# Kernel optimization log

Hardware: AMD Instinct MI355X
Metric: run time of the kernel (lower is better)

The kernel has to match this reference:

```python
import jax, jax.numpy as jnp
import numpy as np

DIM = 512
NUM_HEADS = 8
HEAD_DIM = DIM // NUM_HEADS
LN_EPS = 1e-5


def setup_inputs() -> dict:
    key = jax.random.key(0)
    k1, k2, k3 = jax.random.split(key, 3)
    x = jax.random.normal(k1, (8, DIM, 32, 32), dtype=jnp.float32)
    # torch Linear default init scale ~ 1/sqrt(fan_in); keep values sane
    w_qkv = jax.random.normal(k2, (3 * DIM, DIM), dtype=jnp.float32) * (DIM ** -0.5)
    b_qkv = jax.random.normal(k3, (3 * DIM,), dtype=jnp.float32) * 0.01
    ln_gamma = jnp.ones((DIM,), dtype=jnp.float32)
    ln_beta = jnp.zeros((DIM,), dtype=jnp.float32)
    return {"x": x, "w_qkv": w_qkv, "b_qkv": b_qkv, "ln_gamma": ln_gamma, "ln_beta": ln_beta}


def _rotate_half(t):
    t1, t2 = jnp.split(t, 2, axis=-1)
    return jnp.concatenate((-t2, t1), axis=-1)


def reference(x, w_qkv, b_qkv, ln_gamma, ln_beta):
    B, C, H, W = x.shape
    N = H * W
    nh, hd = NUM_HEADS, HEAD_DIM
    scale = hd ** -0.5

    # [B, N, C]
    xt = x.reshape(B, C, N).transpose(0, 2, 1)

    # LayerNorm over channel dim
    mu = jnp.mean(xt, axis=-1, keepdims=True)
    var = jnp.mean(jnp.square(xt - mu), axis=-1, keepdims=True)
    xn = (xt - mu) * jax.lax.rsqrt(var + LN_EPS) * ln_gamma + ln_beta

    # QKV projection: [B, N, 3C]
    qkv = xn @ w_qkv.T + b_qkv
    qkv = qkv.reshape(B, N, 3, nh, hd).transpose(2, 0, 3, 1, 4)  # [3, B, nh, N, hd]
    q, k, v = qkv[0], qkv[1], qkv[2]

    # RoPE tables
    freqs = 1.0 / (10000.0 ** (jnp.arange(0, hd, 2, dtype=jnp.float32) / hd))
    pos = jnp.arange(N, dtype=jnp.float32)
    sinusoid = jnp.einsum('i,j->ij', pos, freqs)  # [N, hd/2]
    sin = jnp.repeat(jnp.sin(sinusoid), 2, axis=-1)[None, None]  # [1,1,N,hd]
    cos = jnp.repeat(jnp.cos(sinusoid), 2, axis=-1)[None, None]

    q = q * cos + _rotate_half(q) * sin
    k = k * cos + _rotate_half(k) * sin

    # Full softmax attention: [B, nh, N, N]
    attn = jnp.einsum('bhqd,bhkd->bhqk', q, k) * scale
    attn = jax.nn.softmax(attn, axis=-1)
    out = jnp.einsum('bhqk,bhkd->bhqd', attn, v)  # [B, nh, N, hd]

    out = out.transpose(0, 2, 1, 3).reshape(B, N, C)  # [B, N, C]
    # dropout=0 (eval): identity
    return out.transpose(0, 2, 1).reshape(B, C, H, W)
```

## Files before the change

### kernel.cpp

```cpp
#include <hip/hip_runtime.h>
#include <hip/hip_bf16.h>
#include <math.h>

using bf16 = __hip_bfloat16;
typedef __attribute__((ext_vector_type(8))) short short8;
typedef __attribute__((ext_vector_type(4))) float floatx4;
typedef __attribute__((ext_vector_type(4))) unsigned int uint4_;
typedef __attribute__((ext_vector_type(2))) unsigned int uint2_;

#define C_DIM   512
#define N_TOK   1024
#define NHEAD   8
#define HDIM    64
#define LN_EPSF 1e-5f

__device__ __forceinline__ unsigned short f2b(float f) {
    union { float f; unsigned int u; } v; v.f = f;
    unsigned int r = v.u + 0x7FFFu + ((v.u >> 16) & 1u);
    return (unsigned short)(r >> 16);
}
__device__ __forceinline__ float b2f(unsigned short u) {
    union { unsigned int i; float f; } v; v.i = ((unsigned int)u) << 16; return v.f;
}
__device__ __forceinline__ unsigned int cvt_pk_bf16(float lo, float hi) {
    unsigned int r;
    asm("v_cvt_pk_bf16_f32 %0, %1, %2" : "=v"(r) : "v"(lo), "v"(hi));
    return r;
}
__device__ __forceinline__ float fast_exp2(float x) {
    return __builtin_amdgcn_exp2f(x);
}

__global__ __launch_bounds__(256) void lnx_kernel(
        const float* __restrict__ x, const float* __restrict__ w,
        const float* __restrict__ gamma, const float* __restrict__ beta,
        float* __restrict__ sc, unsigned short* __restrict__ wf,
        unsigned short* __restrict__ xnf) {
    __shared__ float xs[C_DIM][36];
    __shared__ float red_s[8][32];
    __shared__ float red_q[8][32];
    __shared__ float muL[32], rsL[32];

    const int bx = blockIdx.x;
    const int t  = threadIdx.x;

    if (bx < 256) {
        const int b  = bx >> 5;
        const int n0 = (bx & 31) * 32;
        const float* xb = x + (size_t)b * C_DIM * N_TOK;

        #pragma unroll
        for (int i = 0; i < 16; ++i) {
            const int flat = i * 256 + t;
            const int c  = flat >> 3;
            const int f4 = flat & 7;
            const float4 v = *(const float4*)(xb + (size_t)c * N_TOK + n0 + f4 * 4);
            *(float4*)&xs[c][f4 * 4] = v;
        }
        __syncthreads();

        const int tl = t & 31, cg = t >> 5;
        float s = 0.f, q = 0.f;
        #pragma unroll 8
        for (int i2 = 0; i2 < 64; ++i2) {
            const float v = xs[cg * 64 + i2][tl];
            s += v; q += v * v;
        }
        red_s[cg][tl] = s; red_q[cg][tl] = q;
        __syncthreads();
        if (t < 32) {
            float S = 0.f, Q = 0.f;
            #pragma unroll
            for (int g2 = 0; g2 < 8; ++g2) { S += red_s[g2][t]; Q += red_q[g2][t]; }
            const float m   = S * (1.0f / C_DIM);
            const float var = Q * (1.0f / C_DIM) - m * m;
            muL[t] = m; rsL[t] = rsqrtf(var + LN_EPSF);
        }
        __syncthreads();

        const int wv   = t >> 6;
        const int lane = t & 63;
        const int cfr  = lane & 15;
        const int quad = lane >> 4;
        #pragma unroll
        for (int gg = 0; gg < 2; ++gg) {
            const int tloc = gg * 16 + cfr;
            const float m = muL[tloc], r = rsL[tloc];
            const int g16 = b * 64 + (n0 >> 4) + gg;
            #pragma unroll
            for (int kk = 0; kk < 4; ++kk) {
                const int kt  = wv * 4 + kk;
                const int ch0 = kt * 32 + quad * 8;
                const float4 g0 = *(const float4*)(gamma + ch0);
                const float4 g1 = *(const float4*)(gamma + ch0 + 4);
                const float4 b0 = *(const float4*)(beta + ch0);
                const float4 b1 = *(const float4*)(beta + ch0 + 4);
                float vv[8];
                #pragma unroll
                for (int j = 0; j < 8; ++j) vv[j] = (xs[ch0 + j][tloc] - m) * r;
                uint4_ pk;
                pk.x = cvt_pk_bf16(vv[0] * g0.x + b0.x, vv[1] * g0.y + b0.y);
                pk.y = cvt_pk_bf16(vv[2] * g0.z + b0.z, vv[3] * g0.w + b0.w);
                pk.z = cvt_pk_bf16(vv[4] * g1.x + b1.x, vv[5] * g1.y + b1.y);
                pk.w = cvt_pk_bf16(vv[6] * g1.z + b1.z, vv[7] * g1.w + b1.w);
                *(uint4_*)(xnf + (((size_t)g16 * 16 + kt) * 64 + lane) * 8) = pk;
            }
        }
    } else if (bx < 384) {
        const int idx = (bx - 256) * 256 + t;
        const int n = idx >> 5, f = idx & 31;
        const float fr = __expf((float)f * (-9.210340371976184f / 32.0f));
        float sv, cv;
        sincosf((float)n * fr, &sv, &cv);
        ((float2*)sc)[idx] = make_float2(sv, cv);
    } else {
        const int id   = (bx - 384) * 256 + t;
        const int lane = id & 63;
        const int ksl  = (id >> 6) & 15;
        const int j16  = id >> 10;
        const int c    = lane & 15;
        const int quad = lane >> 4;
        const float* wp = w + (size_t)(j16 * 16 + c) * C_DIM + ksl * 32 + quad * 8;
        const float4 w0 = *(const float4*)(wp);
        const float4 w1 = *(const float4*)(wp + 4);
        uint4_ pk;
        pk.x = cvt_pk_bf16(w0.x, w0.y);
        pk.y = cvt_pk_bf16(w0.z, w0.w);
        pk.z = cvt_pk_bf16(w1.x, w1.y);
        pk.w = cvt_pk_bf16(w1.z, w1.w);
        *(uint4_*)(wf + (size_t)id * 8) = pk;
    }
}

__global__ __launch_bounds__(256) void qkv_mfma_kernel(
        const unsigned short* __restrict__ xnf, const unsigned short* __restrict__ wf,
        const float* __restrict__ bias, const float* __restrict__ sc,
        unsigned short* __restrict__ qfr, unsigned short* __restrict__ kfr,
        unsigned short* __restrict__ vfr) {
    __shared__ short Es[4][64][72];

    const int t    = threadIdx.x;
    const int wv   = t >> 6;
    const int lane = t & 63;
    const int cl   = lane & 15;
    const int quad = lane >> 4;
    const int t0   = blockIdx.x * 128 + (wv & 1) * 64;
    const int j0w  = blockIdx.y * 128 + (wv >> 1) * 64;
    const int which = j0w >> 9;
    const int h     = (j0w >> 6) & 7;
    const int b     = t0 >> 10;
    const int n0q   = t0 & 1023;
    const int bh    = b * NHEAD + h;

    const unsigned short* ap = xnf + (size_t)(t0 >> 4) * 8192 + lane * 8;
    const unsigned short* bp = wf  + (size_t)(j0w >> 4) * 8192 + lane * 8;

    floatx4 acc[4][4];
    #pragma unroll
    for (int i = 0; i < 4; ++i)
        #pragma unroll
        for (int j = 0; j < 4; ++j) acc[i][j] = (floatx4){0.f, 0.f, 0.f, 0.f};

    #pragma unroll 2
    for (int kt = 0; kt < 16; ++kt) {
        short8 af[4], bfr[4];
        #pragma unroll
        for (int tt = 0; tt < 4; ++tt) af[tt]  = *(const short8*)(ap + ((size_t)tt * 16 + kt) * 512);
        #pragma unroll
        for (int jt = 0; jt < 4; ++jt) bfr[jt] = *(const short8*)(bp + ((size_t)jt * 16 + kt) * 512);
        #pragma unroll
        for (int tt = 0; tt < 4; ++tt)
            #pragma unroll
            for (int jt = 0; jt < 4; ++jt)
                acc[tt][jt] = __builtin_amdgcn_mfma_f32_16x16x32_bf16(af[tt], bfr[jt], acc[tt][jt], 0, 0, 0);
    }

    const float os = (which == 0) ? 0.125f : 1.0f;
    float bj[4];
    #pragma unroll
    for (int jt = 0; jt < 4; ++jt) bj[jt] = bias[j0w + jt * 16 + cl] * os;
    #pragma unroll
    for (int tt = 0; tt < 4; ++tt)
        #pragma unroll
        for (int jt = 0; jt < 4; ++jt)
            #pragma unroll
            for (int r = 0; r < 4; ++r)
                Es[wv][tt * 16 + quad * 4 + r][jt * 16 + cl] = (short)f2b(fmaf(acc[tt][jt][r], os, bj[jt]));

    if (which == 2) {
        unsigned short* vfb = vfr + ((size_t)bh * 16 + (n0q >> 6)) * 4096;
        #pragma unroll
        for (int dt = 0; dt < 4; ++dt) {
            #pragma unroll
            for (int ks = 0; ks < 2; ++ks) {
                short8 pk;
                #pragma unroll
                for (int j = 0; j < 8; ++j)
                    pk[j] = Es[wv][ks * 32 + quad * 8 + j][dt * 16 + cl];
                *(short8*)(vfb + (((size_t)dt * 2 + ks) * 64 + lane) * 8) = pk;
            }
        }
    } else {
        unsigned short* base = (which == 0)
            ? qfr + ((size_t)bh * 64 + (n0q >> 4)) * 1024
            : kfr + ((size_t)bh * 16 + (n0q >> 6)) * 4096;
        #pragma unroll
        for (int mt = 0; mt < 4; ++mt) {
            const int n = n0q + mt * 16 + cl;
            const float* scp = sc + ((size_t)n * 32 + quad * 4) * 2;
            #pragma unroll
            for (int ks = 0; ks < 2; ++ks) {
                const short8 v8 = *(const short8*)&Es[wv][mt * 16 + cl][ks * 32 + quad * 8];
                const short8 p8 = *(const short8*)&Es[wv][mt * 16 + cl][(ks ^ 1) * 32 + quad * 8];
                const float* sp = scp + ks * 32;
                const float4 s0 = *(const float4*)sp;
                const float4 s1 = *(const float4*)(sp + 4);
                const float sv[4] = {s0.x, s0.z, s1.x, s1.z};
                const float cv[4] = {s0.y, s0.w, s1.y, s1.w};
                const float sgn = ks ? 1.0f : -1.0f;
                uint4_ pk;
                unsigned int pw[4];
                #pragma unroll
                for (int f = 0; f < 4; ++f) {
                    const float svs = sgn * sv[f];
                    const float a0 = b2f((unsigned short)v8[2 * f]);
                    const float a1 = b2f((unsigned short)v8[2 * f + 1]);
                    const float p0 = b2f((unsigned short)p8[2 * f]);
                    const float p1 = b2f((unsigned short)p8[2 * f + 1]);
                    pw[f] = cvt_pk_bf16(fmaf(p0, svs, a0 * cv[f]),
                                        fmaf(p1, svs, a1 * cv[f]));
                }
                pk.x = pw[0]; pk.y = pw[1]; pk.z = pw[2]; pk.w = pw[3];
                *(uint4_*)(base + (((size_t)mt * 2 + ks) * 64 + lane) * 8) = pk;
            }
        }
    }
}

__global__ __launch_bounds__(256, 2) void attn_mfma_kernel(
        const unsigned short* __restrict__ qfr, const unsigned short* __restrict__ kfr,
        const unsigned short* __restrict__ vfr, float* __restrict__ out) {
    __shared__ __align__(16) short Plds[4][2][16][72];

    const int t    = threadIdx.x;
    const int wv   = t >> 6;
    const int lane = t & 63;
    const int c    = lane & 15;
    const int quad = lane >> 4;
    const int i    = blockIdx.x;
    const int bh   = (i & 7) * 8 + ((i >> 3) & 7);
    const int q32  = (i >> 6) * 4 + wv;
    const int b    = bh >> 3, h = bh & 7;

    const unsigned short* qp   = qfr + ((size_t)bh * 64 + q32 * 2) * 1024 + lane * 8;
    const unsigned short* kraw = kfr + (size_t)bh * 65536 + lane * 8;
    const unsigned short* vraw = vfr + (size_t)bh * 65536 + lane * 8;

    short8 qf[2][2];
    qf[0][0] = *(const short8*)(qp);
    qf[0][1] = *(const short8*)(qp + 512);
    qf[1][0] = *(const short8*)(qp + 1024);
    qf[1][1] = *(const short8*)(qp + 1536);

    floatx4 o_acc[4][2];
    float l_acc[2] = {0.f, 0.f};
    #pragma unroll
    for (int dt = 0; dt < 4; ++dt) {
        o_acc[dt][0] = (floatx4){0.f, 0.f, 0.f, 0.f};
        o_acc[dt][1] = (floatx4){0.f, 0.f, 0.f, 0.f};
    }

    const float LOG2E  = 1.4426950408889634f;
    const float ESHIFT = -23.083120654223414f;

    short8 kfA[4][2], vfA[4][2], kfB[4][2], vfB[4][2];

    auto loadf = [&](short8 (&kf)[4][2], short8 (&vf)[4][2], int kt) {
        const unsigned short* kc = kraw + (size_t)kt * 4096;
        const unsigned short* vc = vraw + (size_t)kt * 4096;
        #pragma unroll
        for (int mt = 0; mt < 4; ++mt)
            #pragma unroll
            for (int ks = 0; ks < 2; ++ks) {
                kf[mt][ks] = *(const short8*)(kc + (mt * 2 + ks) * 512);
                vf[mt][ks] = *(const short8*)(vc + (mt * 2 + ks) * 512);
            }
    };

    auto step = [&](short8 (&kf)[4][2], short8 (&vf)[4][2]) {
        floatx4 st[4][2];
        __builtin_amdgcn_s_setprio(1);
        #pragma unroll
        for (int mt = 0; mt < 4; ++mt)
            #pragma unroll
            for (int u = 0; u < 2; ++u) {
                floatx4 z = (floatx4){0.f, 0.f, 0.f, 0.f};
                z = __builtin_amdgcn_mfma_f32_16x16x32_bf16(kf[mt][0], qf[u][0], z, 0, 0, 0);
                st[mt][u] = __builtin_amdgcn_mfma_f32_16x16x32_bf16(kf[mt][1], qf[u][1], z, 0, 0, 0);
            }
        __builtin_amdgcn_s_setprio(0);

        #pragma unroll
        for (int u = 0; u < 2; ++u)
            #pragma unroll
            for (int mt = 0; mt < 4; ++mt) {
                const float e0 = fast_exp2(fmaf(st[mt][u][0], LOG2E, ESHIFT));
                const float e1 = fast_exp2(fmaf(st[mt][u][1], LOG2E, ESHIFT));
                const float e2 = fast_exp2(fmaf(st[mt][u][2], LOG2E, ESHIFT));
                const float e3 = fast_exp2(fmaf(st[mt][u][3], LOG2E, ESHIFT));
                l_acc[u] += (e0 + e1) + (e2 + e3);
                uint2_ pk;
                pk.x = cvt_pk_bf16(e0, e1);
                pk.y = cvt_pk_bf16(e2, e3);
                *(uint2_*)&Plds[wv][u][c][mt * 16 + quad * 4] = pk;
            }

        #pragma unroll
        for (int u = 0; u < 2; ++u) {
            const short8 pf0 = *(const short8*)&Plds[wv][u][c][quad * 8];
            const short8 pf1 = *(const short8*)&Plds[wv][u][c][32 + quad * 8];
            __builtin_amdgcn_s_setprio(1);
            #pragma unroll
            for (int dt = 0; dt < 4; ++dt) {
                o_acc[dt][u] = __builtin_amdgcn_mfma_f32_16x16x32_bf16(vf[dt][0], pf0, o_acc[dt][u], 0, 0, 0);
                o_acc[dt][u] = __builtin_amdgcn_mfma_f32_16x16x32_bf16(vf[dt][1], pf1, o_acc[dt][u], 0, 0, 0);
            }
            __builtin_amdgcn_s_setprio(0);
        }
    };

    loadf(kfA, vfA, 0);
    #pragma unroll 1
    for (int kt = 0; kt < 16; kt += 2) {
        loadf(kfB, vfB, kt + 1);
        step(kfA, vfA);
        if (kt + 2 < 16) loadf(kfA, vfA, kt + 2);
        step(kfB, vfB);
    }

    #pragma unroll
    for (int u = 0; u < 2; ++u) {
        float l = l_acc[u];
        l += __shfl_xor(l, 16);
        l += __shfl_xor(l, 32);
        const float inv = 1.0f / l;
        const int qcol = (q32 * 2 + u) * 16 + c;
        #pragma unroll
        for (int dt = 0; dt < 4; ++dt)
            #pragma unroll
            for (int r = 0; r < 4; ++r) {
                const int d = dt * 16 + quad * 4 + r;
                out[((size_t)b * C_DIM + h * HDIM + d) * N_TOK + qcol] = o_acc[dt][u][r] * inv;
            }
    }
}

extern "C" void kernel_launch(void* const* d_in, const int* in_sizes, int n_in,
                              void* d_out, int out_size, void* d_ws, size_t ws_size,
                              hipStream_t stream) {
    const float* x     = (const float*)d_in[0];
    const float* w     = (const float*)d_in[1];
    const float* bias  = (const float*)d_in[2];
    const float* gamma = (const float*)d_in[3];
    const float* beta  = (const float*)d_in[4];
    float* out = (float*)d_out;

    char* ws = (char*)d_ws;
    unsigned short* qfr = (unsigned short*)(ws + 65536);
    unsigned short* kfr = (unsigned short*)(ws + 65536 + 8388608);
    unsigned short* vfr = (unsigned short*)(ws + 65536 + 16777216);
    unsigned short* xnf = (unsigned short*)(ws + 65536 + 25165824);
    unsigned short* wf  = (unsigned short*)(ws + 65536 + 33554432);
    float* sc           = (float*)(ws + 65536 + 35127296);

    hipLaunchKernelGGL(lnx_kernel, dim3(768), dim3(256), 0, stream,
                       x, w, gamma, beta, sc, wf, xnf);
    hipLaunchKernelGGL(qkv_mfma_kernel, dim3(64, 12), dim3(256), 0, stream,
                       xnf, wf, bias, sc, qfr, kfr, vfr);
    hipLaunchKernelGGL(attn_mfma_kernel, dim3(512), dim3(256), 0, stream, qfr, kfr, vfr, out);
}
```

Measured before the change: 125.6 us.

## Stage K/V tiles into LDS via global_load_lds double buffering in attention

The attention kernel previously had every wave load the full K and V fragments for each 64-key tile straight from global memory into registers, so the four waves of a block fetched the same data four times. Now each wave loads a quarter of the tile with direct global-to-LDS loads into a double-buffered shared-memory tile, and all waves read their fragments from LDS, with a block barrier after each tile. This cuts redundant global/L2 traffic and register pressure, but adds LDS reads, more shared memory per block (which may limit occupancy) and per-iteration __syncthreads. The QKV GEMM loop also raises wave priority around its MFMA block.

```diff
diff --git a/kernel.cpp b/kernel.cpp
--- a/kernel.cpp
+++ b/kernel.cpp
@@ -29,6 +29,11 @@
 }
 __device__ __forceinline__ float fast_exp2(float x) {
     return __builtin_amdgcn_exp2f(x);
+}
+typedef __attribute__((address_space(3))) void lds_void;
+typedef const __attribute__((address_space(1))) void gbl_void;
+__device__ __forceinline__ void gl16(const void* g, void* l) {
+    __builtin_amdgcn_global_load_lds((gbl_void*)g, (lds_void*)l, 16, 0, 0);
 }
 
 __global__ __launch_bounds__(256) void lnx_kernel(
@@ -168,11 +173,13 @@
         for (int tt = 0; tt < 4; ++tt) af[tt]  = *(const short8*)(ap + ((size_t)tt * 16 + kt) * 512);
         #pragma unroll
         for (int jt = 0; jt < 4; ++jt) bfr[jt] = *(const short8*)(bp + ((size_t)jt * 16 + kt) * 512);
+        __builtin_amdgcn_s_setprio(1);
         #pragma unroll
         for (int tt = 0; tt < 4; ++tt)
             #pragma unroll
             for (int jt = 0; jt < 4; ++jt)
                 acc[tt][jt] = __builtin_amdgcn_mfma_f32_16x16x32_bf16(af[tt], bfr[jt], acc[tt][jt], 0, 0, 0);
+        __builtin_amdgcn_s_setprio(0);
     }
 
     const float os = (which == 0) ? 0.125f : 1.0f;
@@ -240,6 +247,8 @@
 __global__ __launch_bounds__(256, 2) void attn_mfma_kernel(
         const unsigned short* __restrict__ qfr, const unsigned short* __restrict__ kfr,
         const unsigned short* __restrict__ vfr, float* __restrict__ out) {
+    __shared__ __align__(16) short kbuf[2][4096];
+    __shared__ __align__(16) short vbuf[2][4096];
     __shared__ __align__(16) short Plds[4][2][16][72];
 
     const int t    = threadIdx.x;
@@ -253,8 +262,8 @@
     const int b    = bh >> 3, h = bh & 7;
 
     const unsigned short* qp   = qfr + ((size_t)bh * 64 + q32 * 2) * 1024 + lane * 8;
-    const unsigned short* kraw = kfr + (size_t)bh * 65536 + lane * 8;
-    const unsigned short* vraw = vfr + (size_t)bh * 65536 + lane * 8;
+    const unsigned short* kraw = kfr + (size_t)bh * 65536;
+    const unsigned short* vraw = vfr + (size_t)bh * 65536;
 
     short8 qf[2][2];
     qf[0][0] = *(const short8*)(qp);
@@ -273,32 +282,32 @@
     const float LOG2E  = 1.4426950408889634f;
     const float ESHIFT = -23.083120654223414f;
 
-    short8 kfA[4][2], vfA[4][2], kfB[4][2], vfB[4][2];
-
-    auto loadf = [&](short8 (&kf)[4][2], short8 (&vf)[4][2], int kt) {
+    auto stage = [&](int kt, int cur) {
         const unsigned short* kc = kraw + (size_t)kt * 4096;
         const unsigned short* vc = vraw + (size_t)kt * 4096;
         #pragma unroll
-        for (int mt = 0; mt < 4; ++mt)
-            #pragma unroll
-            for (int ks = 0; ks < 2; ++ks) {
-                kf[mt][ks] = *(const short8*)(kc + (mt * 2 + ks) * 512);
-                vf[mt][ks] = *(const short8*)(vc + (mt * 2 + ks) * 512);
-            }
+        for (int s2 = 0; s2 < 2; ++s2) {
+            const int seg = wv * 2 + s2;
+            gl16(kc + seg * 512 + lane * 8, &kbuf[cur][seg * 512]);
+            gl16(vc + seg * 512 + lane * 8, &vbuf[cur][seg * 512]);
+        }
     };
 
-    auto step = [&](short8 (&kf)[4][2], short8 (&vf)[4][2]) {
+    auto step = [&](int cur) {
         floatx4 st[4][2];
-        __builtin_amdgcn_s_setprio(1);
-        #pragma unroll
-        for (int mt = 0; mt < 4; ++mt)
+        #pragma unroll
+        for (int mt = 0; mt < 4; ++mt) {
+            const short8 k0 = *(const short8*)&kbuf[cur][((mt * 2 + 0) * 64 + lane) * 8];
+            const short8 k1 = *(const short8*)&kbuf[cur][((mt * 2 + 1) * 64 + lane) * 8];
+            __builtin_amdgcn_s_setprio(1);
             #pragma unroll
             for (int u = 0; u < 2; ++u) {
                 floatx4 z = (floatx4){0.f, 0.f, 0.f, 0.f};
-                z = __builtin_amdgcn_mfma_f32_16x16x32_bf16(kf[mt][0], qf[u][0], z, 0, 0, 0);
-                st[mt][u] = __builtin_amdgcn_mfma_f32_16x16x32_bf16(kf[mt][1], qf[u][1], z, 0, 0, 0);
-            }
-        __builtin_amdgcn_s_setprio(0);
+                z = __builtin_amdgcn_mfma_f32_16x16x32_bf16(k0, qf[u][0], z, 0, 0, 0);
+                st[mt][u] = __builtin_amdgcn_mfma_f32_16x16x32_bf16(k1, qf[u][1], z, 0, 0, 0);
+            }
+            __builtin_amdgcn_s_setprio(0);
+        }
 
         #pragma unroll
         for (int u = 0; u < 2; ++u)
@@ -322,20 +331,23 @@
             __builtin_amdgcn_s_setprio(1);
             #pragma unroll
             for (int dt = 0; dt < 4; ++dt) {
-                o_acc[dt][u] = __builtin_amdgcn_mfma_f32_16x16x32_bf16(vf[dt][0], pf0, o_acc[dt][u], 0, 0, 0);
-                o_acc[dt][u] = __builtin_amdgcn_mfma_f32_16x16x32_bf16(vf[dt][1], pf1, o_acc[dt][u], 0, 0, 0);
+                const short8 v0 = *(const short8*)&vbuf[cur][((dt * 2 + 0) * 64 + lane) * 8];
+                const short8 v1 = *(const short8*)&vbuf[cur][((dt * 2 + 1) * 64 + lane) * 8];
+                o_acc[dt][u] = __builtin_amdgcn_mfma_f32_16x16x32_bf16(v0, pf0, o_acc[dt][u], 0, 0, 0);
+                o_acc[dt][u] = __builtin_amdgcn_mfma_f32_16x16x32_bf16(v1, pf1, o_acc[dt][u], 0, 0, 0);
             }
             __builtin_amdgcn_s_setprio(0);
         }
     };
 
-    loadf(kfA, vfA, 0);
+    stage(0, 0);
+    __syncthreads();
     #pragma unroll 1
-    for (int kt = 0; kt < 16; kt += 2) {
-        loadf(kfB, vfB, kt + 1);
-        step(kfA, vfA);
-        if (kt + 2 < 16) loadf(kfA, vfA, kt + 2);
-        step(kfB, vfB);
+    for (int kt = 0; kt < 16; ++kt) {
+        const int cur = kt & 1;
+        if (kt < 15) stage(kt + 1, cur ^ 1);
+        step(cur);
+        __syncthreads();
     }
 
     #pragma unroll
```

New measurement: 127.0 us. About the same (+1.1%).

## Double-buffer QKV GEMM operands via async global-to-LDS loads; fuse LN stats into load

Applied to the files above, without the earlier changes.

The QKV MFMA kernel now stages the A and B fragment tiles for each k-step into a double-buffered LDS region using global_load_lds. Each tile is loaded once per block and shared by the waves, rather than every wave reading it from global memory, and the next k-step's load overlaps the current MFMAs. MFMA sections are wrapped in s_setprio. LDS is reused for the epilogue staging. Separately, the LayerNorm kernel accumulates sums and sums of squares while loading x and reduces them with warp shuffles, replacing a second pass over shared memory. The price is a block barrier on every k-step and unroll 1.

```diff
diff --git a/kernel.cpp b/kernel.cpp
--- a/kernel.cpp
+++ b/kernel.cpp
@@ -29,6 +29,11 @@
 }
 __device__ __forceinline__ float fast_exp2(float x) {
     return __builtin_amdgcn_exp2f(x);
+}
+typedef __attribute__((address_space(3))) void lds_void;
+typedef const __attribute__((address_space(1))) void gbl_void;
+__device__ __forceinline__ void gl16(const void* g, void* l) {
+    __builtin_amdgcn_global_load_lds((gbl_void*)g, (lds_void*)l, 16, 0, 0);
 }
 
 __global__ __launch_bounds__(256) void lnx_kernel(
@@ -37,8 +42,8 @@
         float* __restrict__ sc, unsigned short* __restrict__ wf,
         unsigned short* __restrict__ xnf) {
     __shared__ float xs[C_DIM][36];
-    __shared__ float red_s[8][32];
-    __shared__ float red_q[8][32];
+    __shared__ float redw_s[4][8][4];
+    __shared__ float redw_q[4][8][4];
     __shared__ float muL[32], rsL[32];
 
     const int bx = blockIdx.x;
@@ -49,6 +54,7 @@
         const int n0 = (bx & 31) * 32;
         const float* xb = x + (size_t)b * C_DIM * N_TOK;
 
+        float s4[4] = {0.f, 0.f, 0.f, 0.f}, q4[4] = {0.f, 0.f, 0.f, 0.f};
         #pragma unroll
         for (int i = 0; i < 16; ++i) {
             const int flat = i * 256 + t;
@@ -56,30 +62,40 @@
             const int f4 = flat & 7;
             const float4 v = *(const float4*)(xb + (size_t)c * N_TOK + n0 + f4 * 4);
             *(float4*)&xs[c][f4 * 4] = v;
-        }
-        __syncthreads();
-
-        const int tl = t & 31, cg = t >> 5;
-        float s = 0.f, q = 0.f;
-        #pragma unroll 8
-        for (int i2 = 0; i2 < 64; ++i2) {
-            const float v = xs[cg * 64 + i2][tl];
-            s += v; q += v * v;
-        }
-        red_s[cg][tl] = s; red_q[cg][tl] = q;
+            s4[0] += v.x; q4[0] += v.x * v.x;
+            s4[1] += v.y; q4[1] += v.y * v.y;
+            s4[2] += v.z; q4[2] += v.z * v.z;
+            s4[3] += v.w; q4[3] += v.w * v.w;
+        }
+        #pragma unroll
+        for (int m = 8; m <= 32; m <<= 1)
+            #pragma unroll
+            for (int j = 0; j < 4; ++j) {
+                s4[j] += __shfl_xor(s4[j], m);
+                q4[j] += __shfl_xor(q4[j], m);
+            }
+        const int wv = t >> 6, lane = t & 63;
+        if (lane < 8) {
+            #pragma unroll
+            for (int j = 0; j < 4; ++j) {
+                redw_s[wv][lane][j] = s4[j];
+                redw_q[wv][lane][j] = q4[j];
+            }
+        }
         __syncthreads();
         if (t < 32) {
             float S = 0.f, Q = 0.f;
             #pragma unroll
-            for (int g2 = 0; g2 < 8; ++g2) { S += red_s[g2][t]; Q += red_q[g2][t]; }
+            for (int w2 = 0; w2 < 4; ++w2) {
+                S += redw_s[w2][t >> 2][t & 3];
+                Q += redw_q[w2][t >> 2][t & 3];
+            }
             const float m   = S * (1.0f / C_DIM);
             const float var = Q * (1.0f / C_DIM) - m * m;
             muL[t] = m; rsL[t] = rsqrtf(var + LN_EPSF);
         }
         __syncthreads();
 
-        const int wv   = t >> 6;
-        const int lane = t & 63;
         const int cfr  = lane & 15;
         const int quad = lane >> 4;
         #pragma unroll
@@ -137,23 +153,38 @@
         const float* __restrict__ bias, const float* __restrict__ sc,
         unsigned short* __restrict__ qfr, unsigned short* __restrict__ kfr,
         unsigned short* __restrict__ vfr) {
-    __shared__ short Es[4][64][72];
+    __shared__ __align__(16) char smem[36864];
+    short* stg = (short*)smem;
+    short (*Es)[72] = (short(*)[72])smem;
 
     const int t    = threadIdx.x;
     const int wv   = t >> 6;
     const int lane = t & 63;
     const int cl   = lane & 15;
     const int quad = lane >> 4;
-    const int t0   = blockIdx.x * 128 + (wv & 1) * 64;
-    const int j0w  = blockIdx.y * 128 + (wv >> 1) * 64;
+    const int tb   = blockIdx.x * 128;
+    const int jb   = blockIdx.y * 128;
+    const int t0   = tb + (wv & 1) * 64;
+    const int j0w  = jb + (wv >> 1) * 64;
     const int which = j0w >> 9;
     const int h     = (j0w >> 6) & 7;
     const int b     = t0 >> 10;
     const int n0q   = t0 & 1023;
     const int bh    = b * NHEAD + h;
-
-    const unsigned short* ap = xnf + (size_t)(t0 >> 4) * 8192 + lane * 8;
-    const unsigned short* bp = wf  + (size_t)(j0w >> 4) * 8192 + lane * 8;
+    const int g16b  = tb >> 4;
+    const int j16b  = jb >> 4;
+
+    auto stage = [&](int kt, int cur) {
+        short* dst = stg + cur * 8192;
+        #pragma unroll
+        for (int s = 0; s < 4; ++s) {
+            const int id = wv * 4 + s;
+            const unsigned short* src = (id < 8)
+                ? xnf + (size_t)(g16b + id) * 8192 + kt * 512 + lane * 8
+                : wf  + (size_t)(j16b + (id - 8)) * 8192 + kt * 512 + lane * 8;
+            gl16(src, dst + id * 512);
+        }
+    };
 
     floatx4 acc[4][4];
     #pragma unroll
@@ -161,19 +192,29 @@
         #pragma unroll
         for (int j = 0; j < 4; ++j) acc[i][j] = (floatx4){0.f, 0.f, 0.f, 0.f};
 
-    #pragma unroll 2
+    stage(0, 0);
+    #pragma unroll 1
     for (int kt = 0; kt < 16; ++kt) {
+        const int cur = kt & 1;
+        __syncthreads();
+        if (kt < 15) stage(kt + 1, cur ^ 1);
+        const short* base = stg + cur * 8192;
         short8 af[4], bfr[4];
         #pragma unroll
-        for (int tt = 0; tt < 4; ++tt) af[tt]  = *(const short8*)(ap + ((size_t)tt * 16 + kt) * 512);
-        #pragma unroll
-        for (int jt = 0; jt < 4; ++jt) bfr[jt] = *(const short8*)(bp + ((size_t)jt * 16 + kt) * 512);
+        for (int tt = 0; tt < 4; ++tt)
+            af[tt]  = *(const short8*)(base + ((wv & 1) * 4 + tt) * 512 + lane * 8);
+        #pragma unroll
+        for (int jt = 0; jt < 4; ++jt)
+            bfr[jt] = *(const short8*)(base + (8 + (wv >> 1) * 4 + jt) * 512 + lane * 8);
+        __builtin_amdgcn_s_setprio(1);
         #pragma unroll
         for (int tt = 0; tt < 4; ++tt)
             #pragma unroll
             for (int jt = 0; jt < 4; ++jt)
                 acc[tt][jt] = __builtin_amdgcn_mfma_f32_16x16x32_bf16(af[tt], bfr[jt], acc[tt][jt], 0, 0, 0);
-    }
+        __builtin_amdgcn_s_setprio(0);
+    }
+    __syncthreads();
 
     const float os = (which == 0) ? 0.125f : 1.0f;
     float bj[4];
@@ -185,7 +226,7 @@
         for (int jt = 0; jt < 4; ++jt)
             #pragma unroll
             for (int r = 0; r < 4; ++r)
-                Es[wv][tt * 16 + quad * 4 + r][jt * 16 + cl] = (short)f2b(fmaf(acc[tt][jt][r], os, bj[jt]));
+                Es[wv * 64 + tt * 16 + quad * 4 + r][jt * 16 + cl] = (short)f2b(fmaf(acc[tt][jt][r], os, bj[jt]));
 
     if (which == 2) {
         unsigned short* vfb = vfr + ((size_t)bh * 16 + (n0q >> 6)) * 4096;
@@ -196,7 +237,7 @@
                 short8 pk;
                 #pragma unroll
                 for (int j = 0; j < 8; ++j)
-                    pk[j] = Es[wv][ks * 32 + quad * 8 + j][dt * 16 + cl];
+                    pk[j] = Es[wv * 64 + ks * 32 + quad * 8 + j][dt * 16 + cl];
                 *(short8*)(vfb + (((size_t)dt * 2 + ks) * 64 + lane) * 8) = pk;
             }
         }
@@ -210,8 +251,8 @@
             const float* scp = sc + ((size_t)n * 32 + quad * 4) * 2;
             #pragma unroll
             for (int ks = 0; ks < 2; ++ks) {
-                const short8 v8 = *(const short8*)&Es[wv][mt * 16 + cl][ks * 32 + quad * 8];
-                const short8 p8 = *(const short8*)&Es[wv][mt * 16 + cl][(ks ^ 1) * 32 + quad * 8];
+                const short8 v8 = *(const short8*)&Es[wv * 64 + mt * 16 + cl][ks * 32 + quad * 8];
+                const short8 p8 = *(const short8*)&Es[wv * 64 + mt * 16 + cl][(ks ^ 1) * 32 + quad * 8];
                 const float* sp = scp + ks * 32;
                 const float4 s0 = *(const float4*)sp;
                 const float4 s1 = *(const float4*)(sp + 4);
```

Measured after the change: 126.0 us. About the same (+0.2%).
